# Performance work log

Hardware: AMD Instinct MI355X
Metric: run time of the kernel (lower is better)

The kernel has to match this reference:

```python
import jax, jax.numpy as jnp
import numpy as np

EPS = 1e-12
LORA_RANK = 16

def setup_inputs() -> dict:
    key = jax.random.key(0)
    ks = jax.random.split(key, 7)
    bs, sq, din, dout = 8, 2048, 2048, 2048
    n_tasks, n_splits, n_skills, r = 32, 1, 8, LORA_RANK
    return {
        'x': jax.random.normal(ks[0], (bs, sq, din), dtype=jnp.float32),
        'W': jax.random.normal(ks[1], (dout, din), dtype=jnp.float32) * (1.0 / np.sqrt(din)),
        'b': jax.random.normal(ks[2], (dout,), dtype=jnp.float32) * 0.02,
        'module_logits': jax.random.normal(ks[3], (n_tasks, n_splits * n_skills), dtype=jnp.float32) * 0.001,
        'A': jax.random.normal(ks[4], (n_splits, n_skills, din // n_splits, r), dtype=jnp.float32) * 0.02,
        'B': jax.random.normal(ks[5], (n_splits, n_skills, r, dout // n_splits), dtype=jnp.float32) * 0.02,
        'tasks': jax.random.randint(ks[6], (bs,), 0, n_tasks),
    }

def reference(x, W, b, module_logits, A, B, tasks):
    bs, sq, din = x.shape
    n_splits, n_skills, _, r = A.shape
    dout = W.shape[0]
    # Polytropon selector (eval mode): sigmoid + normalize over skills
    probs = jax.nn.sigmoid(module_logits[tasks]).reshape(bs, n_splits, n_skills)
    probs = probs / (probs.sum(-1, keepdims=True) + EPS)  # [bs, p, t]
    # WeightedSum combinor: per-example skill mixture of LoRA params
    A_c = jnp.einsum('bpt,ptir->bpir', probs, A)  # [bs, p, din/p, r]
    B_c = jnp.einsum('bpt,ptro->bpro', probs, B)  # [bs, p, r, dout/p]
    # LoRA forward: reshape to per-example [din, r] and [r, dout]
    A_r = A_c.reshape(bs, din, r)
    B_r = jnp.transpose(B_c, (0, 2, 1, 3)).reshape(bs, r, dout)
    lora = jnp.einsum('bsr,bro->bso', jnp.einsum('bsi,bir->bsr', x, A_r), B_r)
    base = jnp.einsum('bsi,oi->bso', x, W) + b
    return base + lora * (1.0 / r)
```

## Files before the change

kernel.cpp:

```cpp
#include <hip/hip_runtime.h>

typedef __attribute__((ext_vector_type(4))) float f32x4;
typedef __attribute__((ext_vector_type(8))) short bf16x8;

__device__ __forceinline__ unsigned short f2b(float f) {
  unsigned u = __float_as_uint(f);
  u = (u + 0x7FFFu + ((u >> 16) & 1u)) >> 16;
  return (unsigned short)u;
}

#define BAR() asm volatile("s_barrier" ::: "memory")
#define VMCNT(N) asm volatile("s_waitcnt vmcnt(" #N ")" ::: "memory")

__global__ void combine_kernel(const float* __restrict__ logits,
                               const int*   __restrict__ tasks,
                               const float* __restrict__ A,
                               const float* __restrict__ B,
                               unsigned short* __restrict__ Art,
                               unsigned short* __restrict__ Brt)
{
  int idx = blockIdx.x * 256 + threadIdx.x;
  int b = idx >> 11;
  int i = idx & 2047;
  if (b >= 8) return;
  int task = tasks[b];
  float p[8]; float s = 0.f;
  #pragma unroll
  for (int t = 0; t < 8; ++t) {
    float l = logits[task * 8 + t];
    float e = 1.f / (1.f + __expf(-l));
    p[t] = e; s += e;
  }
  float inv = 1.f / (s + 1e-12f);
  #pragma unroll
  for (int t = 0; t < 8; ++t) p[t] *= inv;

  float ar[16];
  #pragma unroll
  for (int r = 0; r < 16; ++r) ar[r] = 0.f;
  for (int t = 0; t < 8; ++t) {
    const float* ap = A + ((size_t)t * 2048 + i) * 16;
    float pt = p[t];
    #pragma unroll
    for (int r = 0; r < 16; ++r) ar[r] += pt * ap[r];
  }
  #pragma unroll
  for (int r = 0; r < 16; ++r)
    Art[((size_t)b * 16 + r) * 2048 + i] = f2b(ar[r]);

  float br[16];
  #pragma unroll
  for (int r = 0; r < 16; ++r) br[r] = 0.f;
  for (int t = 0; t < 8; ++t) {
    float pt = p[t];
    #pragma unroll
    for (int r = 0; r < 16; ++r) br[r] += pt * B[((size_t)t * 16 + r) * 2048 + i];
  }
  #pragma unroll
  for (int r = 0; r < 16; ++r)
    Brt[((size_t)b * 2048 + i) * 16 + r] = f2b(br[r] * 0.0625f);
}

__global__ void wconv_kernel(const float* __restrict__ W, unsigned short* __restrict__ Wb) {
  size_t i = ((size_t)blockIdx.x * 256 + threadIdx.x) * 4;
  f32x4 v = *(const f32x4*)(W + i);
  ushort4 o;
  o.x = f2b(v.x); o.y = f2b(v.y); o.z = f2b(v.z); o.w = f2b(v.w);
  *(ushort4*)(Wb + i) = o;
}

__global__ void xa_conv_kernel(const float* __restrict__ x,
                               const unsigned short* __restrict__ Art,
                               unsigned short* __restrict__ xb,
                               unsigned short* __restrict__ xa)
{
  __shared__ unsigned short As[64 * 64];
  int tid = threadIdx.x;
  int lane = tid & 63;
  int wv = tid >> 6;
  int rowbase = blockIdx.x * 64;
  int batch = rowbase >> 11;
  int lr = lane & 15, hi = lane >> 4;
  f32x4 acc; acc.x = 0.f; acc.y = 0.f; acc.z = 0.f; acc.w = 0.f;

  for (int k0 = 0; k0 < 2048; k0 += 64) {
    #pragma unroll
    for (int p = 0; p < 4; ++p) {
      int row = p * 16 + (tid >> 4);
      int k = (tid & 15) * 4;
      f32x4 v = *(const f32x4*)(x + (size_t)(rowbase + row) * 2048 + k0 + k);
      ushort4 o;
      o.x = f2b(v.x); o.y = f2b(v.y); o.z = f2b(v.z); o.w = f2b(v.w);
      *(ushort4*)(xb + (size_t)(rowbase + row) * 2048 + k0 + k) = o;
      *(ushort4*)(As + row * 64 + k) = o;
    }
    __syncthreads();
    #pragma unroll
    for (int kk = 0; kk < 64; kk += 32) {
      bf16x8 a = *(const bf16x8*)(As + (wv * 16 + lr) * 64 + kk + hi * 8);
      bf16x8 bf = *(const bf16x8*)(Art + ((size_t)batch * 16 + lr) * 2048 + k0 + kk + hi * 8);
      acc = __builtin_amdgcn_mfma_f32_16x16x32_bf16(a, bf, acc, 0, 0, 0);
    }
    __syncthreads();
  }
  #pragma unroll
  for (int j = 0; j < 4; ++j) {
    int row = rowbase + wv * 16 + hi * 4 + j;
    xa[(size_t)row * 16 + lr] = f2b(acc[j]);
  }
}

__global__ __launch_bounds__(512, 2)
void gemm_kernel(const unsigned short* __restrict__ xb,
                 const unsigned short* __restrict__ Wb,
                 const float* __restrict__ bias,
                 const unsigned short* __restrict__ xa,
                 const unsigned short* __restrict__ Brt,
                 float* __restrict__ out)
{
  __shared__ __align__(16) char lds[131072];
  const int tid = threadIdx.x;
  const int lane = tid & 63;
  const int wv = tid >> 6;
  const int wr = wv >> 2, wc = wv & 3;
  const int lr = lane & 15, hi = lane >> 4;
  const int hi16 = hi * 16;

  const int bid = blockIdx.x;
  const int swz = (bid & 7) * 64 + (bid >> 3);
  const int tm = swz >> 3, tn = swz & 7;
  const int rowbase = tm * 256, colbase = tn * 256;

  const int row0 = tid >> 3;
  const int cb0 = (tid & 7) * 16;
  const int scb_e = (cb0 ^ ((row0 & 7) << 4)) >> 1;
  const int rb5 = ((row0 >> 5) << 6) + (row0 & 31);

#define GL16(LDSOFF, GPTR) \
  __builtin_amdgcn_global_load_lds((const __attribute__((address_space(1))) unsigned int*)(GPTR), \
      (__attribute__((address_space(3))) unsigned int*)(lds + (LDSOFF)), 16, 0, 0)

#define STAGE_A(MH, DBUF, KOFF) { \
  const unsigned short* g_ = xb + (size_t)(rowbase + (MH)*64 + row0) * 2048 + (KOFF) + scb_e; \
  GL16((DBUF)*65536 + (MH)*16384 + tid*16, g_); \
  GL16((DBUF)*65536 + (MH)*16384 + 8192 + tid*16, g_ + 128*2048); \
}
#define STAGE_B(NH, DBUF, KOFF) { \
  const unsigned short* g_ = Wb + (size_t)(colbase + (NH)*32 + rb5) * 2048 + (KOFF) + scb_e; \
  GL16((DBUF)*65536 + 32768 + (NH)*16384 + tid*16, g_); \
  GL16((DBUF)*65536 + 32768 + (NH)*16384 + 8192 + tid*16, g_ + 128*2048); \
}

#define READ_A(MH) \
  _Pragma("unroll") \
  for (int mf = 0; mf < 4; ++mf) { \
    int ar_ = (MH)*128 + wr*64 + mf*16 + lr; \
    _Pragma("unroll") \
    for (int kk = 0; kk < 2; ++kk) \
      a[mf][kk] = *(const bf16x8*)(Ab + ar_*128 + ((kk*64 + hi16) ^ ((ar_&7)<<4))); \
  }
#define READ_B(NH, BREG) \
  _Pragma("unroll") \
  for (int nf = 0; nf < 2; ++nf) { \
    int br_ = (NH)*128 + wc*32 + nf*16 + lr; \
    _Pragma("unroll") \
    for (int kk = 0; kk < 2; ++kk) \
      BREG[nf][kk] = *(const bf16x8*)(Bb + br_*128 + ((kk*64 + hi16) ^ ((br_&7)<<4))); \
  }
#define MFMA_BLOCK(MH, NH, BREG) \
  __builtin_amdgcn_s_setprio(1); \
  _Pragma("unroll") \
  for (int mf = 0; mf < 4; ++mf) \
    _Pragma("unroll") \
    for (int nf = 0; nf < 2; ++nf) \
      _Pragma("unroll") \
      for (int kk = 0; kk < 2; ++kk) \
        acc[(MH)*4+mf][(NH)*2+nf] = __builtin_amdgcn_mfma_f32_16x16x32_bf16( \
            a[mf][kk], BREG[nf][kk], acc[(MH)*4+mf][(NH)*2+nf], 0, 0, 0); \
  __builtin_amdgcn_s_setprio(0);

  f32x4 acc[8][4];
  #pragma unroll
  for (int i = 0; i < 8; ++i)
    #pragma unroll
    for (int n = 0; n < 4; ++n) { acc[i][n].x = 0.f; acc[i][n].y = 0.f; acc[i][n].z = 0.f; acc[i][n].w = 0.f; }

  bf16x8 a[4][2], b0[2][2], b1[2][2];

  STAGE_A(0, 0, 0);
  STAGE_B(0, 0, 0);
  STAGE_A(1, 0, 0);
  STAGE_B(1, 0, 0);
  STAGE_A(0, 1, 64);
  STAGE_B(0, 1, 64);
  VMCNT(4);
  BAR();

  for (int kt = 0; kt < 32; ++kt) {
    const int buf = kt & 1, nbuf = buf ^ 1;
    const char* Ab = lds + buf * 65536;
    const char* Bb = Ab + 32768;
    const int k1 = (kt + 1) * 64, k2 = (kt + 2) * 64;

    READ_A(0);
    READ_B(0, b0);
    if (kt < 31) STAGE_A(1, nbuf, k1);
    BAR();
    MFMA_BLOCK(0, 0, b0);
    if (kt < 31) { VMCNT(3); } else { VMCNT(0); }
    BAR();

    READ_B(1, b1);
    if (kt < 31) STAGE_B(1, nbuf, k1);
    BAR();
    MFMA_BLOCK(0, 1, b1);
    BAR();

    READ_A(1);
    if (kt < 30) STAGE_A(0, buf, k2);
    BAR();
    MFMA_BLOCK(1, 0, b0);
    BAR();

    if (kt < 30) STAGE_B(0, buf, k2);
    BAR();
    MFMA_BLOCK(1, 1, b1);
    if (kt < 30) { VMCNT(4); }
    else if (kt == 30) { VMCNT(2); }
    BAR();
  }

  const int batch = rowbase >> 11;
  bf16x8 zf = (bf16x8)(short)0;
  bf16x8 av[8], bv[4];
  #pragma unroll
  for (int i = 0; i < 8; ++i) {
    if (hi < 2)
      av[i] = *(const bf16x8*)(xa + (size_t)(rowbase + wr * 128 + i * 16 + lr) * 16 + hi * 8);
    else
      av[i] = zf;
  }
  #pragma unroll
  for (int n = 0; n < 4; ++n) {
    if (hi < 2)
      bv[n] = *(const bf16x8*)(Brt + ((size_t)batch * 2048 + colbase + wc * 64 + n * 16 + lr) * 16 + hi * 8);
    else
      bv[n] = zf;
  }
  #pragma unroll
  for (int i = 0; i < 8; ++i)
    #pragma unroll
    for (int n = 0; n < 4; ++n)
      acc[i][n] = __builtin_amdgcn_mfma_f32_16x16x32_bf16(av[i], bv[n], acc[i][n], 0, 0, 0);

  #pragma unroll
  for (int n = 0; n < 4; ++n) {
    int col = colbase + wc * 64 + n * 16 + lr;
    float bbv = bias[col];
    #pragma unroll
    for (int i = 0; i < 8; ++i) {
      int r0 = rowbase + wr * 128 + i * 16 + hi * 4;
      #pragma unroll
      for (int j = 0; j < 4; ++j)
        out[(size_t)(r0 + j) * 2048 + col] = acc[i][n][j] + bbv;
    }
  }
#undef GL16
#undef STAGE_A
#undef STAGE_B
#undef READ_A
#undef READ_B
#undef MFMA_BLOCK
}

extern "C" void kernel_launch(void* const* d_in, const int* in_sizes, int n_in,
                              void* d_out, int out_size, void* d_ws, size_t ws_size,
                              hipStream_t stream) {
  const float* x      = (const float*)d_in[0];
  const float* W      = (const float*)d_in[1];
  const float* bias   = (const float*)d_in[2];
  const float* logits = (const float*)d_in[3];
  const float* A      = (const float*)d_in[4];
  const float* B      = (const float*)d_in[5];
  const int*   tasks  = (const int*)d_in[6];
  float* out = (float*)d_out;

  char* ws = (char*)d_ws;
  unsigned short* xb  = (unsigned short*)(ws);
  unsigned short* Wb  = (unsigned short*)(ws + 67108864);
  unsigned short* xa  = (unsigned short*)(ws + 67108864 + 8388608);
  unsigned short* Art = (unsigned short*)(ws + 67108864 + 8388608 + 524288);
  unsigned short* Brt = (unsigned short*)(ws + 67108864 + 8388608 + 1048576);

  combine_kernel<<<64, 256, 0, stream>>>(logits, tasks, A, B, Art, Brt);
  wconv_kernel<<<4096, 256, 0, stream>>>(W, Wb);
  xa_conv_kernel<<<256, 256, 0, stream>>>(x, Art, xb, xa);
  gemm_kernel<<<512, 512, 0, stream>>>(xb, Wb, bias, xa, Brt, out);
}
```

Baseline: 206.5 us.

## Merge W and x conversion kernels into one prep kernel and relax GEMM waitcnts

```diff
diff --git a/kernel.cpp b/kernel.cpp
--- a/kernel.cpp
+++ b/kernel.cpp
@@ -61,53 +61,56 @@
     Brt[((size_t)b * 2048 + i) * 16 + r] = f2b(br[r] * 0.0625f);
 }
 
-__global__ void wconv_kernel(const float* __restrict__ W, unsigned short* __restrict__ Wb) {
-  size_t i = ((size_t)blockIdx.x * 256 + threadIdx.x) * 4;
-  f32x4 v = *(const f32x4*)(W + i);
-  ushort4 o;
-  o.x = f2b(v.x); o.y = f2b(v.y); o.z = f2b(v.z); o.w = f2b(v.w);
-  *(ushort4*)(Wb + i) = o;
-}
-
-__global__ void xa_conv_kernel(const float* __restrict__ x,
-                               const unsigned short* __restrict__ Art,
-                               unsigned short* __restrict__ xb,
-                               unsigned short* __restrict__ xa)
+__global__ void prep_kernel(const float* __restrict__ x,
+                            const unsigned short* __restrict__ Art,
+                            const float* __restrict__ W,
+                            unsigned short* __restrict__ Wb,
+                            unsigned short* __restrict__ xb,
+                            unsigned short* __restrict__ xa)
 {
-  __shared__ unsigned short As[64 * 64];
+  __shared__ float red[4][16][16];
+  int blk = blockIdx.x;
   int tid = threadIdx.x;
-  int lane = tid & 63;
-  int wv = tid >> 6;
-  int rowbase = blockIdx.x * 64;
-  int batch = rowbase >> 11;
-  int lr = lane & 15, hi = lane >> 4;
-  f32x4 acc; acc.x = 0.f; acc.y = 0.f; acc.z = 0.f; acc.w = 0.f;
-
-  for (int k0 = 0; k0 < 2048; k0 += 64) {
-    #pragma unroll
-    for (int p = 0; p < 4; ++p) {
-      int row = p * 16 + (tid >> 4);
-      int k = (tid & 15) * 4;
-      f32x4 v = *(const f32x4*)(x + (size_t)(rowbase + row) * 2048 + k0 + k);
+  if (blk >= 1024) {
+    int idx0 = (blk - 1024) * 256 + tid;
+    #pragma unroll
+    for (int c = 0; c < 32; ++c) {
+      size_t i = ((size_t)idx0 + (size_t)c * 32768) * 4;
+      f32x4 v = *(const f32x4*)(W + i);
       ushort4 o;
       o.x = f2b(v.x); o.y = f2b(v.y); o.z = f2b(v.z); o.w = f2b(v.w);
-      *(ushort4*)(xb + (size_t)(rowbase + row) * 2048 + k0 + k) = o;
-      *(ushort4*)(As + row * 64 + k) = o;
+      *(ushort4*)(Wb + i) = o;
     }
-    __syncthreads();
-    #pragma unroll
-    for (int kk = 0; kk < 64; kk += 32) {
-      bf16x8 a = *(const bf16x8*)(As + (wv * 16 + lr) * 64 + kk + hi * 8);
-      bf16x8 bf = *(const bf16x8*)(Art + ((size_t)batch * 16 + lr) * 2048 + k0 + kk + hi * 8);
-      acc = __builtin_amdgcn_mfma_f32_16x16x32_bf16(a, bf, acc, 0, 0, 0);
-    }
-    __syncthreads();
-  }
-  #pragma unroll
-  for (int j = 0; j < 4; ++j) {
-    int row = rowbase + wv * 16 + hi * 4 + j;
-    xa[(size_t)row * 16 + lr] = f2b(acc[j]);
-  }
+    return;
+  }
+  int lane = tid & 63, wv = tid >> 6;
+  int lr = lane & 15, hi = lane >> 4;
+  int rowbase = blk * 16;
+  int batch = rowbase >> 11;
+  int row = rowbase + lr;
+  f32x4 acc; acc.x = 0.f; acc.y = 0.f; acc.z = 0.f; acc.w = 0.f;
+  const float* xrow = x + (size_t)row * 2048 + wv * 512 + hi * 8;
+  unsigned short* xbrow = xb + (size_t)row * 2048 + wv * 512 + hi * 8;
+  const unsigned short* artrow = Art + ((size_t)batch * 16 + lr) * 2048 + wv * 512 + hi * 8;
+  #pragma unroll
+  for (int ks = 0; ks < 16; ++ks) {
+    f32x4 v0 = *(const f32x4*)(xrow + ks * 32);
+    f32x4 v1 = *(const f32x4*)(xrow + ks * 32 + 4);
+    bf16x8 av;
+    av[0] = (short)f2b(v0.x); av[1] = (short)f2b(v0.y);
+    av[2] = (short)f2b(v0.z); av[3] = (short)f2b(v0.w);
+    av[4] = (short)f2b(v1.x); av[5] = (short)f2b(v1.y);
+    av[6] = (short)f2b(v1.z); av[7] = (short)f2b(v1.w);
+    *(bf16x8*)(xbrow + ks * 32) = av;
+    bf16x8 bv = *(const bf16x8*)(artrow + ks * 32);
+    acc = __builtin_amdgcn_mfma_f32_16x16x32_bf16(av, bv, acc, 0, 0, 0);
+  }
+  #pragma unroll
+  for (int j = 0; j < 4; ++j) red[wv][hi * 4 + j][lr] = acc[j];
+  __syncthreads();
+  int rr = tid >> 4, cc = tid & 15;
+  float s = red[0][rr][cc] + red[1][rr][cc] + red[2][rr][cc] + red[3][rr][cc];
+  xa[(size_t)(rowbase + rr) * 16 + cc] = f2b(s);
 }
 
 __global__ __launch_bounds__(512, 2)
@@ -193,7 +196,7 @@
   STAGE_B(1, 0, 0);
   STAGE_A(0, 1, 64);
   STAGE_B(0, 1, 64);
-  VMCNT(4);
+  VMCNT(8);
   BAR();
 
   for (int kt = 0; kt < 32; ++kt) {
@@ -207,7 +210,7 @@
     if (kt < 31) STAGE_A(1, nbuf, k1);
     BAR();
     MFMA_BLOCK(0, 0, b0);
-    if (kt < 31) { VMCNT(3); } else { VMCNT(0); }
+    if (kt < 31) { VMCNT(6); } else { VMCNT(0); }
     BAR();
 
     READ_B(1, b1);
@@ -225,8 +228,8 @@
     if (kt < 30) STAGE_B(0, buf, k2);
     BAR();
     MFMA_BLOCK(1, 1, b1);
-    if (kt < 30) { VMCNT(4); }
-    else if (kt == 30) { VMCNT(2); }
+    if (kt < 30) { VMCNT(6); }
+    else if (kt == 30) { VMCNT(4); }
     BAR();
   }
 
@@ -293,7 +296,6 @@
   unsigned short* Brt = (unsigned short*)(ws + 67108864 + 8388608 + 1048576);
 
   combine_kernel<<<64, 256, 0, stream>>>(logits, tasks, A, B, Art, Brt);
-  wconv_kernel<<<4096, 256, 0, stream>>>(W, Wb);
-  xa_conv_kernel<<<256, 256, 0, stream>>>(x, Art, xb, xa);
+  prep_kernel<<<1152, 256, 0, stream>>>(x, Art, W, Wb, xb, xa);
   gemm_kernel<<<512, 512, 0, stream>>>(xb, Wb, bias, xa, Brt, out);
 }
```

Result: faster. 193.3 us (-6.4%).
